# Kernel optimization log

Measured on AMD Instinct MI355X. Metric: run time of the kernel, lower is better.

The kernel has to match this reference:

```python
import jax, jax.numpy as jnp
import numpy as np

POSTFIX = jnp.array([[1.0, 0.0, 1.0, 0.0],
                     [0.0, 1.0, 0.0, 1.0],
                     [-0.5, 0.0, 0.5, 0.0],
                     [0.0, -0.5, 0.0, 0.5]], dtype=jnp.float32)


def roi_pool(feat, rois_scaled, out_h=16, out_w=8):
    # feat: [B,C,H,W]; rois_scaled: [B,4] float (x1,y1,x2,y2 in pixel units).
    # Faithful to torch: rois.long() truncation, slice y1:y2+1 / x1:x2+1 (end clipped
    # to H/W), then F.adaptive_max_pool2d with PyTorch bin boundaries
    # start=floor(i*h/out), end=ceil((i+1)*h/out).
    H, W = feat.shape[2], feat.shape[3]
    r = rois_scaled.astype(jnp.int32)  # values are >= 0 after clamp, trunc == floor

    def one(f, ri):  # f: [C,H,W], ri: [4] int32
        x1, y1 = ri[0], ri[1]
        x2 = jnp.minimum(ri[2], W - 1)  # slice end clipping
        y2 = jnp.minimum(ri[3], H - 1)
        h = y2 - y1 + 1
        w = x2 - x1 + 1
        # column bins
        j = jnp.arange(out_w)
        cs = x1 + (j * w) // out_w
        ce = x1 + ((j + 1) * w + out_w - 1) // out_w  # ceil
        cols = jnp.arange(W)
        cmask = (cols[None, :] >= cs[:, None]) & (cols[None, :] < ce[:, None])  # [out_w,W]
        t = jnp.max(jnp.where(cmask[:, None, None, :], f[None], -jnp.inf), axis=3)  # [out_w,C,H]
        # row bins
        i = jnp.arange(out_h)
        rs = y1 + (i * h) // out_h
        re = y1 + ((i + 1) * h + out_h - 1) // out_h
        rows = jnp.arange(H)
        rmask = (rows[None, :] >= rs[:, None]) & (rows[None, :] < re[:, None])  # [out_h,H]
        out = jnp.max(jnp.where(rmask[:, None, None, :], t[None], -jnp.inf), axis=3)  # [out_h,out_w,C]
        return jnp.transpose(out, (2, 0, 1))  # [C,out_h,out_w]

    return jax.vmap(one)(feat, r)


def setup_inputs() -> dict:
    key = jax.random.key(0)
    ks = jax.random.split(key, 12)
    B = 16
    return {
        "box_xywh": jax.random.uniform(ks[0], (B, 4), dtype=jnp.float32),
        "x2": jax.random.normal(ks[1], (B, 64, 128, 128), dtype=jnp.float32),
        "x4": jax.random.normal(ks[2], (B, 160, 64, 64), dtype=jnp.float32),
        "x6": jax.random.normal(ks[3], (B, 192, 32, 32), dtype=jnp.float32),
        "Wh": jax.random.normal(ks[4], (7, 53248, 128), dtype=jnp.float32) * 0.01,
        "bh": jax.random.normal(ks[5], (7, 128), dtype=jnp.float32) * 0.01,
        "Wp": jax.random.normal(ks[6], (128, 38), dtype=jnp.float32) * 0.05,
        "bp": jax.random.normal(ks[7], (38,), dtype=jnp.float32) * 0.05,
        "Wa": jax.random.normal(ks[8], (128, 25), dtype=jnp.float32) * 0.05,
        "ba": jax.random.normal(ks[9], (25,), dtype=jnp.float32) * 0.05,
        "Wd": jax.random.normal(ks[10], (5, 128, 35), dtype=jnp.float32) * 0.05,
        "bd": jax.random.normal(ks[11], (5, 35), dtype=jnp.float32) * 0.05,
    }


def reference(box_xywh, x2, x4, x6, Wh, bh, Wp, bp, Wa, ba, Wd, bd):
    B = box_xywh.shape[0]
    box_xyxy = jnp.clip(box_xywh @ POSTFIX, 0.0, 1.0)  # [B,4]
    # Faithful to original: x coords scaled by size(2)=H, y coords by size(3)=W.
    def scale(feat):
        H, W = feat.shape[2], feat.shape[3]
        return box_xyxy * jnp.array([H, W, H, W], dtype=box_xyxy.dtype)
    p1 = roi_pool(x2, scale(x2))   # [B,64,16,8]
    p2 = roi_pool(x4, scale(x4))   # [B,160,16,8]
    p3 = roi_pool(x6, scale(x6))   # [B,192,16,8]
    rois = jnp.concatenate([p1, p2, p3], axis=1).reshape(B, -1)  # [B,53248]
    hid = jnp.einsum('bf,kfh->kbh', rois, Wh) + bh[:, None, :]   # [7,B,128]
    o1 = hid[0] @ Wp + bp                                        # [B,38]
    o2 = hid[1] @ Wa + ba                                        # [B,25]
    od = jnp.einsum('kbh,kho->bko', hid[2:], Wd) + bd[None]      # [B,5,35]
    return jnp.concatenate([box_xywh, o1, o2, od.reshape(B, -1)], axis=1)  # [B,242]
```

## Files before the change

### kernel.cpp

```cpp
#include <hip/hip_runtime.h>
#include <math.h>


#define B 16
#define F_TOT 53248
#define FC 512
#define NCHUNK (F_TOT / FC)

__device__ __forceinline__ float clamp01(float v) {
    return fminf(fmaxf(v, 0.0f), 1.0f);
}

__global__ __launch_bounds__(256) void roi_all(const float* __restrict__ x2,
                                               const float* __restrict__ x4,
                                               const float* __restrict__ x6,
                                               const float* __restrict__ box,
                                               float* __restrict__ rois) {
    const int blk = blockIdx.x;
    const float* feat;
    int C, S, fbase, t;
    if (blk < 512)       { feat = x2; C = 64;  S = 128; fbase = 0;     t = blk * 256 + threadIdx.x; }
    else if (blk < 1792) { feat = x4; C = 160; S = 64;  fbase = 8192;  t = (blk - 512) * 256 + threadIdx.x; }
    else                 { feat = x6; C = 192; S = 32;  fbase = 28672; t = (blk - 1792) * 256 + threadIdx.x; }

    int j = t & 7;
    int i = (t >> 3) & 15;
    int c = (t >> 7) % C;
    int b = t / (C << 7);

    const float* bx = box + b * 4;
    float x = bx[0], y = bx[1], wd = bx[2], ht = bx[3];
    float Sf = (float)S;
    int x1 = (int)(clamp01(x - 0.5f * wd) * Sf);
    int y1 = (int)(clamp01(y - 0.5f * ht) * Sf);
    int x2i = (int)(clamp01(x + 0.5f * wd) * Sf);
    int y2i = (int)(clamp01(y + 0.5f * ht) * Sf);
    x2i = min(x2i, S - 1);
    y2i = min(y2i, S - 1);
    int h = y2i - y1 + 1;
    int w = x2i - x1 + 1;

    int rs = y1 + (i * h) / 16;
    int re = y1 + ((i + 1) * h + 15) / 16;
    int cs = x1 + (j * w) / 8;
    int ce = x1 + ((j + 1) * w + 7) / 8;

    const float* fp = feat + ((size_t)(b * C + c)) * S * S;
    float m = -INFINITY;
    for (int r = rs; r < re; ++r) {
        const float* row = fp + r * S;
        for (int cc = cs; cc < ce; ++cc) m = fmaxf(m, row[cc]);
    }
    int f = fbase + (c * 16 + i) * 8 + j;
    rois[(size_t)b * F_TOT + f] = m;
}

__global__ __launch_bounds__(256) void matmul_part(const float* __restrict__ rois,
                                                   const float* __restrict__ Wh,
                                                   float* __restrict__ partial) {
    __shared__ float rs_[FC * 16];
    const int cid = blockIdx.x;
    const int k = blockIdx.y;
    const int f0 = cid * FC;
    const int tid = threadIdx.x;

    for (int idx = tid; idx < FC * 16; idx += 256) {
        int b = idx & 15;
        int fl = idx >> 4;
        rs_[idx] = rois[(size_t)b * F_TOT + f0 + fl];
    }
    __syncthreads();

    const int w    = tid >> 6;
    const int l    = tid & 63;
    const int half = l >> 5;
    const int h0   = (l & 31) * 4;

    const float* wp = Wh + ((size_t)k * F_TOT + f0 + 2 * w + half) * 128 + h0;
    int fb = ((2 * w + half) << 4);

    float4 acc[16];
#pragma unroll
    for (int b = 0; b < 16; ++b) acc[b] = make_float4(0.f, 0.f, 0.f, 0.f);

#pragma unroll 4
    for (int it = 0; it < FC / 8; ++it) {
        const float4 wv = *(const float4*)wp;
        wp += 8 * 128;
        const float* rp = rs_ + fb;
        fb += 128;
#pragma unroll
        for (int q = 0; q < 4; ++q) {
            const float4 rv = *(const float4*)(rp + q * 4);
            acc[q*4+0].x += rv.x * wv.x; acc[q*4+0].y += rv.x * wv.y;
            acc[q*4+0].z += rv.x * wv.z; acc[q*4+0].w += rv.x * wv.w;
            acc[q*4+1].x += rv.y * wv.x; acc[q*4+1].y += rv.y * wv.y;
            acc[q*4+1].z += rv.y * wv.z; acc[q*4+1].w += rv.y * wv.w;
            acc[q*4+2].x += rv.z * wv.x; acc[q*4+2].y += rv.z * wv.y;
            acc[q*4+2].z += rv.z * wv.z; acc[q*4+2].w += rv.z * wv.w;
            acc[q*4+3].x += rv.w * wv.x; acc[q*4+3].y += rv.w * wv.y;
            acc[q*4+3].z += rv.w * wv.z; acc[q*4+3].w += rv.w * wv.w;
        }
    }

    __syncthreads();
    float* red = rs_;
    if (half == 0) {
#pragma unroll
        for (int b = 0; b < 16; ++b)
            *(float4*)(red + w * 2048 + b * 128 + h0) = acc[b];
    }
    __syncthreads();
    if (half == 1) {
#pragma unroll
        for (int b = 0; b < 16; ++b) {
            float4* p = (float4*)(red + w * 2048 + b * 128 + h0);
            float4 t = *p;
            t.x += acc[b].x; t.y += acc[b].y; t.z += acc[b].z; t.w += acc[b].w;
            *p = t;
        }
    }
    __syncthreads();

    float* op = partial + ((size_t)(k * NCHUNK + cid)) * (B * 128);
    for (int idx = tid; idx < 2048; idx += 256) {
        op[idx] = red[idx] + red[idx + 2048] + red[idx + 4096] + red[idx + 6144];
    }
}

__global__ __launch_bounds__(512) void tail_kernel(const float* __restrict__ partial,
                                                   const float* __restrict__ bh,
                                                   const float* __restrict__ box,
                                                   const float* __restrict__ Wp, const float* __restrict__ bp,
                                                   const float* __restrict__ Wa, const float* __restrict__ ba,
                                                   const float* __restrict__ Wd, const float* __restrict__ bd,
                                                   float* __restrict__ out) {
    __shared__ float red[512];
    __shared__ float hs[128];
    const int k = blockIdx.x >> 4;
    const int b = blockIdx.x & 15;
    const int tid = threadIdx.x;

    {
        const int h = tid & 127;
        const int q = tid >> 7;
        const float* pp = partial + (size_t)k * NCHUNK * (B * 128) + b * 128 + h
                        + (size_t)(q * 26) * (B * 128);
        float s = 0.f;
#pragma unroll
        for (int cid = 0; cid < 26; ++cid) s += pp[(size_t)cid * (B * 128)];
        red[tid] = s;
    }
    __syncthreads();
    if (tid < 128) {
        hs[tid] = red[tid] + red[tid + 128] + red[tid + 256] + red[tid + 384]
                + bh[k * 128 + tid];
    }
    __syncthreads();

    const int o = tid >> 3;
    const int p = tid & 7;
    const int n_out = (k == 0) ? 38 : (k == 1) ? 25 : 35;
    float v = 0.f;
    if (o < n_out) {
        const float* Wc;
        int ld;
        if (k == 0)      { Wc = Wp; ld = 38; }
        else if (k == 1) { Wc = Wa; ld = 25; }
        else             { Wc = Wd + (size_t)(k - 2) * 128 * 35; ld = 35; }
        const int hbase = p * 16;
#pragma unroll
        for (int hh = 0; hh < 16; ++hh) {
            const int h = hbase + hh;
            v += hs[h] * Wc[h * ld + o];
        }
    }
    v += __shfl_xor(v, 1, 8);
    v += __shfl_xor(v, 2, 8);
    v += __shfl_xor(v, 4, 8);
    if (p == 0 && o < n_out) {
        float bias;
        int off;
        if (k == 0)      { bias = bp[o]; off = 4 + o; }
        else if (k == 1) { bias = ba[o]; off = 42 + o; }
        else             { bias = bd[(k - 2) * 35 + o]; off = 67 + (k - 2) * 35 + o; }
        out[b * 242 + off] = bias + v;
    }
    if (k == 0 && tid >= 504) {
        const int j = tid - 504;
        if (j < 4) out[b * 242 + j] = box[b * 4 + j];
    }
}

extern "C" void kernel_launch(void* const* d_in, const int* in_sizes, int n_in,
                              void* d_out, int out_size, void* d_ws, size_t ws_size,
                              hipStream_t stream) {
    const float* box = (const float*)d_in[0];
    const float* x2  = (const float*)d_in[1];
    const float* x4  = (const float*)d_in[2];
    const float* x6  = (const float*)d_in[3];
    const float* Wh  = (const float*)d_in[4];
    const float* bh  = (const float*)d_in[5];
    const float* Wp  = (const float*)d_in[6];
    const float* bp  = (const float*)d_in[7];
    const float* Wa  = (const float*)d_in[8];
    const float* ba  = (const float*)d_in[9];
    const float* Wd  = (const float*)d_in[10];
    const float* bd  = (const float*)d_in[11];
    float* out = (float*)d_out;

    float* ws = (float*)d_ws;
    float* rois    = ws;
    float* partial = ws + (size_t)B * F_TOT;

    roi_all<<<3328, 256, 0, stream>>>(x2, x4, x6, box, rois);
    matmul_part<<<dim3(NCHUNK, 7), 256, 0, stream>>>(rois, Wh, partial);
    tail_kernel<<<112, 512, 0, stream>>>(partial, bh, box, Wp, bp, Wa, ba, Wd, bd, out);
}
```

Baseline: 370.4 us.

## Store ROI features batch-interleaved, vectorize staging, use nontemporal weight loads

The ROI pooling kernel now maps batch to the fastest-varying thread index and writes pooled features in a feature-major, batch-interleaved layout. The matmul kernel can then stage its chunk into shared memory with contiguous float4 copies instead of a strided gather. The column max loop is unrolled by four, and the large Wh weight stream is read with nontemporal loads to avoid polluting cache. As a trade-off, neighbouring threads in the pooling kernel now read different images, which scatters feature-map reads across batches.

Result: faster. 353.3 us (-4.6%).

```diff
diff --git a/kernel.cpp b/kernel.cpp
--- a/kernel.cpp
+++ b/kernel.cpp
@@ -6,6 +6,8 @@
 #define F_TOT 53248
 #define FC 512
 #define NCHUNK (F_TOT / FC)
+
+typedef float vf4 __attribute__((ext_vector_type(4)));
 
 __device__ __forceinline__ float clamp01(float v) {
     return fminf(fmaxf(v, 0.0f), 1.0f);
@@ -23,10 +25,11 @@
     else if (blk < 1792) { feat = x4; C = 160; S = 64;  fbase = 8192;  t = (blk - 512) * 256 + threadIdx.x; }
     else                 { feat = x6; C = 192; S = 32;  fbase = 28672; t = (blk - 1792) * 256 + threadIdx.x; }
 
-    int j = t & 7;
-    int i = (t >> 3) & 15;
-    int c = (t >> 7) % C;
-    int b = t / (C << 7);
+    const int b = t & 15;
+    const int f = t >> 4;
+    const int j = f & 7;
+    const int i = (f >> 3) & 15;
+    const int c = f >> 7;
 
     const float* bx = box + b * 4;
     float x = bx[0], y = bx[1], wd = bx[2], ht = bx[3];
@@ -49,10 +52,17 @@
     float m = -INFINITY;
     for (int r = rs; r < re; ++r) {
         const float* row = fp + r * S;
-        for (int cc = cs; cc < ce; ++cc) m = fmaxf(m, row[cc]);
-    }
-    int f = fbase + (c * 16 + i) * 8 + j;
-    rois[(size_t)b * F_TOT + f] = m;
+        int cc = cs;
+        for (; cc + 3 < ce; cc += 4) {
+            float a0 = row[cc + 0];
+            float a1 = row[cc + 1];
+            float a2 = row[cc + 2];
+            float a3 = row[cc + 3];
+            m = fmaxf(m, fmaxf(fmaxf(a0, a1), fmaxf(a2, a3)));
+        }
+        for (; cc < ce; ++cc) m = fmaxf(m, row[cc]);
+    }
+    rois[(size_t)blk * 256 + threadIdx.x] = m;
 }
 
 __global__ __launch_bounds__(256) void matmul_part(const float* __restrict__ rois,
@@ -64,10 +74,10 @@
     const int f0 = cid * FC;
     const int tid = threadIdx.x;
 
-    for (int idx = tid; idx < FC * 16; idx += 256) {
-        int b = idx & 15;
-        int fl = idx >> 4;
-        rs_[idx] = rois[(size_t)b * F_TOT + f0 + fl];
+    {
+        const float4* src = (const float4*)(rois + (size_t)f0 * 16);
+        float4* dst = (float4*)rs_;
+        for (int idx = tid; idx < FC * 16 / 4; idx += 256) dst[idx] = src[idx];
     }
     __syncthreads();
 
@@ -85,7 +95,7 @@
 
 #pragma unroll 4
     for (int it = 0; it < FC / 8; ++it) {
-        const float4 wv = *(const float4*)wp;
+        const vf4 wv = __builtin_nontemporal_load((const vf4*)wp);
         wp += 8 * 128;
         const float* rp = rs_ + fb;
         fb += 128;
@@ -212,6 +222,7 @@
     float* ws = (float*)d_ws;
     float* rois    = ws;
     float* partial = ws + (size_t)B * F_TOT;
+    (void)ws_size;
 
     roi_all<<<3328, 256, 0, stream>>>(x2, x4, x6, box, rois);
     matmul_part<<<dim3(NCHUNK, 7), 256, 0, stream>>>(rois, Wh, partial);
```
